# Optimization experiments

Hardware: AMD Instinct MI355X
Metric: run time of the kernel (lower is better)

Reference implementation:

```python
import jax, jax.numpy as jnp
import numpy as np

H2 = 512    # internal hidden = hidden_size*2
E = 128     # embedding_size
V = 50000   # vocabulary_size
L = 512     # max_length (encoder input length)
B = 128     # batch


def setup_inputs() -> dict:
    key = jax.random.key(0)
    ks = jax.random.split(key, 20)
    s = 0.02
    return {
        "input_ids": jax.random.randint(ks[0], (B,), 0, V),
        "hidden": jax.random.normal(ks[1], (1, B, H2), jnp.float32),
        "encoder_outputs": jax.random.normal(ks[2], (L, B, H2), jnp.float32),
        "full_input": jax.random.randint(ks[3], (L, B), 0, V),
        # parameters
        "embedding": jax.random.normal(ks[4], (V, E), jnp.float32) * s,
        "W_ih": jax.random.normal(ks[5], (3 * H2, E), jnp.float32) * s,
        "W_hh": jax.random.normal(ks[6], (3 * H2, H2), jnp.float32) * s,
        "b_ih": jnp.zeros((3 * H2,), jnp.float32),
        "b_hh": jnp.zeros((3 * H2,), jnp.float32),
        "W_ds": jax.random.normal(ks[7], (H2, H2), jnp.float32) * s,
        "b_ds": jnp.zeros((H2,), jnp.float32),
        "w_h": jax.random.normal(ks[8], (H2,), jnp.float32),
        "att_v": jax.random.normal(ks[9], (H2,), jnp.float32),
        "W_oh": jax.random.normal(ks[10], (E, 2 * H2), jnp.float32) * s,
        "b_oh": jnp.zeros((E,), jnp.float32),
        "W_ov": jax.random.normal(ks[11], (V, E), jnp.float32) * s,
        "b_ov": jnp.zeros((V,), jnp.float32),
        "W_ptr": jax.random.normal(ks[12], (1, 2 * H2 + E), jnp.float32) * s,
        "b_ptr": jnp.zeros((1,), jnp.float32),
    }


def reference(input_ids, hidden, encoder_outputs, full_input, embedding,
              W_ih, W_hh, b_ih, b_hh, W_ds, b_ds, w_h, att_v,
              W_oh, b_oh, W_ov, b_ov, W_ptr, b_ptr):
    Bn = input_ids.shape[0]
    Ln = encoder_outputs.shape[0]
    Vn = embedding.shape[0]

    emb = embedding[input_ids]                       # [B, E] (dropout = identity in eval)
    h0 = hidden[0]                                   # [B, 2h]

    # single GRU step (PyTorch gate order r, z, n)
    gx = emb @ W_ih.T + b_ih                         # [B, 3*2h]
    gh = h0 @ W_hh.T + b_hh
    xr, xz, xn = jnp.split(gx, 3, axis=1)
    hr, hz, hn = jnp.split(gh, 3, axis=1)
    r = jax.nn.sigmoid(xr + hr)
    z = jax.nn.sigmoid(xz + hz)
    n = jnp.tanh(xn + r * hn)
    h_new = (1.0 - z) * n + z * h0                   # [B, 2h]

    # Bahdanau-style attention (faithful to source, incl. softmax over dim=1 = batch axis)
    dsl = h_new @ W_ds.T + b_ds                      # [B, 2h]
    att = jnp.tanh(w_h * encoder_outputs + dsl[None])  # [L, B, 2h]
    scores = (att_v * att).sum(-1)                   # [L, B]
    attn = jax.nn.softmax(scores, axis=1)            # torch F.softmax(dim=1)

    context = jnp.einsum('lb,lbh->bh', attn, encoder_outputs)  # [B, 2h]
    combined = jnp.concatenate([h_new, context], axis=1)        # [B, 4h]

    p_vocab = jax.nn.softmax((combined @ W_oh.T + b_oh) @ W_ov.T + b_ov, axis=1)  # [B, V]

    p_gen = jax.nn.sigmoid(jnp.concatenate([combined, emb], axis=1) @ W_ptr.T + b_ptr)  # [B, 1]

    # scatter attention mass onto extended vocab (copy distribution)
    token_input_dist = jnp.zeros((Bn, Vn + Ln), p_vocab.dtype).at[
        jnp.arange(Bn)[:, None], full_input.T
    ].add(attn.T)

    pad = jnp.zeros((Bn, Ln), p_vocab.dtype)
    p_final = jnp.concatenate([p_vocab * p_gen, pad], axis=1) + (1.0 - p_gen) * token_input_dist
    return (p_final, h_new[None], attn)
```

## Files before the change

### kernel.cpp

```cpp
#include <hip/hip_runtime.h>
#include <math.h>

#define B_  128
#define E_  128
#define H2_ 512
#define H3_ 1536
#define L_  512
#define V_  50000
#define VL_ 50512

typedef short bf16x8 __attribute__((ext_vector_type(8)));
typedef float f32x4 __attribute__((ext_vector_type(4)));

__device__ __forceinline__ float fast_tanh(float x) {
    float e = __expf(2.f * x);
    return 1.f - 2.f / (e + 1.f);
}
__device__ __forceinline__ float fast_sigmoid(float x) {
    return 1.f / (1.f + __expf(-x));
}
__device__ __forceinline__ short f2bf(float f) {
    unsigned u = __float_as_uint(f);
    u += 0x7fff + ((u >> 16) & 1);
    return (short)(u >> 16);
}

__global__ void k_init(float* __restrict__ gx, float* __restrict__ gh,
                       float* __restrict__ dsl, float* __restrict__ hid,
                       float* __restrict__ out, float* __restrict__ rsum8,
                       const float* __restrict__ b_ih, const float* __restrict__ b_hh,
                       const float* __restrict__ b_ds, const float* __restrict__ b_oh) {
    int i = blockIdx.x * blockDim.x + threadIdx.x;
    if (i < 196608) { gx[i] = b_ih[i % 1536]; return; }
    i -= 196608;
    if (i < 196608) { gh[i] = b_hh[i % 1536]; return; }
    i -= 196608;
    if (i < 65536)  { dsl[i] = b_ds[i & 511]; return; }
    i -= 65536;
    if (i < 16384)  { hid[i] = b_oh[i & 127]; return; }
    i -= 16384;
    if (i < 65536)  { out[(size_t)(i >> 9) * VL_ + V_ + (i & 511)] = 0.f; return; }
    i -= 65536;
    if (i < 1024)   rsum8[i] = 0.f;
}

__global__ void k_gates(const int* __restrict__ ids, const float* __restrict__ tab,
                        const float* __restrict__ hidden,
                        const float* __restrict__ W_ih, const float* __restrict__ W_hh,
                        float* __restrict__ gx, float* __restrict__ gh) {
    __shared__ float As[32][36];
    __shared__ float Ws[32][36];
    int z = blockIdx.z;
    int which = (z < 2) ? 0 : 1;
    int kbeg  = which ? (z - 2) * 128 : z * 64;
    int kiter = which ? 4 : 2;
    const float* W = which ? W_hh : W_ih;
    int ldw = which ? H2_ : E_;
    float* C = which ? gh : gx;
    int bm = blockIdx.x * 32, bn = blockIdx.y * 32;
    int tid = threadIdx.x;
    int tm0 = (tid / 16) * 2, tn0 = (tid % 16) * 2;
    float acc[2][2] = {};
    for (int it = 0; it < kiter; ++it) {
        int k0 = kbeg + it * 32;
        for (int v = tid; v < 256; v += 256) {
            int m = v >> 3, q = (v & 7) << 2;
            int gm = bm + m;
            const float* arow = which ? (hidden + (size_t)gm * H2_)
                                      : (tab + (size_t)ids[gm] * E_);
            float4 x = *(const float4*)(arow + k0 + q);
            As[q+0][m] = x.x; As[q+1][m] = x.y; As[q+2][m] = x.z; As[q+3][m] = x.w;
        }
        for (int v = tid; v < 256; v += 256) {
            int n = v >> 3, q = (v & 7) << 2;
            float4 x = *(const float4*)(W + (size_t)(bn + n) * ldw + k0 + q);
            Ws[q+0][n] = x.x; Ws[q+1][n] = x.y; Ws[q+2][n] = x.z; Ws[q+3][n] = x.w;
        }
        __syncthreads();
        #pragma unroll
        for (int kk = 0; kk < 32; ++kk) {
            float a0 = As[kk][tm0], a1 = As[kk][tm0+1];
            float w0 = Ws[kk][tn0], w1 = Ws[kk][tn0+1];
            acc[0][0] += a0*w0; acc[0][1] += a0*w1;
            acc[1][0] += a1*w0; acc[1][1] += a1*w1;
        }
        __syncthreads();
    }
    #pragma unroll
    for (int i = 0; i < 2; ++i)
        #pragma unroll
        for (int j = 0; j < 2; ++j)
            atomicAdd(&C[(size_t)(bm+tm0+i) * H3_ + bn+tn0+j], acc[i][j]);
}

template<int BM, int BN, int BK, int TM, int TN, int SPLITK>
__global__ void gemm_t(const float* __restrict__ A, int lda,
                       const float* __restrict__ W, int ldw,
                       float* __restrict__ C, int ldc,
                       int N, int K) {
    __shared__ float As[BK][BM + 4];
    __shared__ float Ws[BK][BN + 4];
    int bm = blockIdx.x * BM, bn = blockIdx.y * BN;
    int tid = threadIdx.x;
    constexpr int NT = BN / TN;
    int tm0 = (tid / NT) * TM;
    int tn0 = (tid % NT) * TN;
    int kchunk = K / SPLITK;
    int kbeg = blockIdx.z * kchunk;
    float acc[TM][TN] = {};
    for (int k0 = kbeg; k0 < kbeg + kchunk; k0 += BK) {
        #pragma unroll
        for (int v = tid; v < BM * BK / 4; v += 256) {
            int m = v / (BK / 4), q = (v % (BK / 4)) * 4;
            float4 x = *(const float4*)(A + (size_t)(bm + m) * lda + k0 + q);
            As[q+0][m] = x.x; As[q+1][m] = x.y; As[q+2][m] = x.z; As[q+3][m] = x.w;
        }
        #pragma unroll
        for (int v = tid; v < BN * BK / 4; v += 256) {
            int n = v / (BK / 4), q = (v % (BK / 4)) * 4;
            float4 x = *(const float4*)(W + (size_t)(bn + n) * ldw + k0 + q);
            Ws[q+0][n] = x.x; Ws[q+1][n] = x.y; Ws[q+2][n] = x.z; Ws[q+3][n] = x.w;
        }
        __syncthreads();
        #pragma unroll
        for (int kk = 0; kk < BK; ++kk) {
            float a[TM], w[TN];
            #pragma unroll
            for (int i = 0; i < TM; ++i) a[i] = As[kk][tm0 + i];
            #pragma unroll
            for (int j = 0; j < TN; ++j) w[j] = Ws[kk][tn0 + j];
            #pragma unroll
            for (int i = 0; i < TM; ++i)
                #pragma unroll
                for (int j = 0; j < TN; ++j) acc[i][j] += a[i] * w[j];
        }
        __syncthreads();
    }
    #pragma unroll
    for (int i = 0; i < TM; ++i)
        #pragma unroll
        for (int j = 0; j < TN; ++j)
            atomicAdd(&C[(size_t)(bm+tm0+i) * ldc + bn+tn0+j], acc[i][j]);
}

__global__ void k_gru(const float* __restrict__ gx, const float* __restrict__ gh,
                      const float* __restrict__ h0,
                      float* __restrict__ comb, float* __restrict__ hout) {
    int idx = blockIdx.x * blockDim.x + threadIdx.x;
    int b = idx >> 9, h = idx & 511;
    const float* gxb = gx + b * H3_;
    const float* ghb = gh + b * H3_;
    float xr = gxb[h], xz = gxb[H2_ + h], xn = gxb[2 * H2_ + h];
    float hr = ghb[h], hz = ghb[H2_ + h], hn = ghb[2 * H2_ + h];
    float r = fast_sigmoid(xr + hr);
    float z = fast_sigmoid(xz + hz);
    float n = fast_tanh(xn + r * hn);
    float hv = (1.f - z) * n + z * h0[idx];
    comb[b * (2 * H2_) + h] = hv;
    comb[b * (2 * H2_) + H2_ + h] = 0.f;
    hout[idx] = hv;
}

__global__ void k_scores(const float* __restrict__ enc, const float* __restrict__ dsl,
                         const float* __restrict__ w_h, const float* __restrict__ att_v,
                         float* __restrict__ scores) {
    int wid = (blockIdx.x << 2) + (threadIdx.x >> 6);
    int lane = threadIdx.x & 63;
    int b = wid & 127, lg = wid >> 7;
    int l0 = lg << 3;
    const float4* d4 = (const float4*)(dsl + b * H2_);
    const float4* w4 = (const float4*)w_h;
    const float4* v4 = (const float4*)att_v;
    float4 d0 = d4[lane], d1 = d4[lane + 64];
    float4 w0 = w4[lane], w1 = w4[lane + 64];
    float4 v0 = v4[lane], v1 = v4[lane + 64];
    float4 e0[8], e1[8];
    #pragma unroll
    for (int q = 0; q < 8; ++q) {
        const float4* e4 = (const float4*)(enc + ((size_t)((l0 + q) * B_ + b)) * H2_);
        e0[q] = e4[lane];
        e1[q] = e4[lane + 64];
    }
    float s[8];
    #pragma unroll
    for (int q = 0; q < 8; ++q) {
        float t;
        t  = v0.x * fast_tanh(w0.x * e0[q].x + d0.x);
        t += v0.y * fast_tanh(w0.y * e0[q].y + d0.y);
        t += v0.z * fast_tanh(w0.z * e0[q].z + d0.z);
        t += v0.w * fast_tanh(w0.w * e0[q].w + d0.w);
        t += v1.x * fast_tanh(w1.x * e1[q].x + d1.x);
        t += v1.y * fast_tanh(w1.y * e1[q].y + d1.y);
        t += v1.z * fast_tanh(w1.z * e1[q].z + d1.z);
        t += v1.w * fast_tanh(w1.w * e1[q].w + d1.w);
        s[q] = t;
    }
    #pragma unroll
    for (int q = 0; q < 8; ++q) {
        float t = s[q];
        #pragma unroll
        for (int o = 32; o; o >>= 1) t += __shfl_xor(t, o);
        if (lane == 0) scores[(l0 + q) * B_ + b] = t;
    }
}

__global__ void k_softmax(const float* __restrict__ scores, float* __restrict__ attn) {
    int l = blockIdx.x, lane = threadIdx.x;
    float s0 = scores[l * B_ + lane], s1 = scores[l * B_ + lane + 64];
    float m = fmaxf(s0, s1);
    #pragma unroll
    for (int o = 32; o; o >>= 1) m = fmaxf(m, __shfl_xor(m, o));
    float e0 = __expf(s0 - m), e1 = __expf(s1 - m);
    float t = e0 + e1;
    #pragma unroll
    for (int o = 32; o; o >>= 1) t += __shfl_xor(t, o);
    float inv = 1.f / t;
    attn[l * B_ + lane] = e0 * inv;
    attn[l * B_ + lane + 64] = e1 * inv;
}

__global__ void k_context(const float* __restrict__ enc, const float* __restrict__ attn,
                          float* __restrict__ comb) {
    int b = blockIdx.x;
    int l0 = blockIdx.y << 6;
    int tid = threadIdx.x;
    __shared__ float a_s[64];
    if (tid < 64) a_s[tid] = attn[(l0 + tid) * B_ + b];
    __syncthreads();
    const float4* e = (const float4*)(enc + ((size_t)l0 * B_ + b) * H2_) + tid;
    float4 c = make_float4(0.f, 0.f, 0.f, 0.f);
    #pragma unroll 8
    for (int i = 0; i < 64; ++i) {
        float4 x = e[(size_t)i * (B_ * H2_ / 4)];
        float a = a_s[i];
        c.x += a * x.x; c.y += a * x.y; c.z += a * x.z; c.w += a * x.w;
    }
    float* dst = comb + b * (2 * H2_) + H2_ + tid * 4;
    atomicAdd(dst + 0, c.x); atomicAdd(dst + 1, c.y);
    atomicAdd(dst + 2, c.z); atomicAdd(dst + 3, c.w);
}

__global__ void k_pgen(const float* __restrict__ comb,
                       const int* __restrict__ ids, const float* __restrict__ tab,
                       const float* __restrict__ W_ptr, const float* __restrict__ b_ptr,
                       float* __restrict__ pgen) {
    int b = blockIdx.x, lane = threadIdx.x;
    float s = 0.f;
    for (int j = lane; j < 2 * H2_; j += 64) s += W_ptr[j] * comb[b * (2 * H2_) + j];
    const float* erow = tab + (size_t)ids[b] * E_;
    for (int j = lane; j < E_; j += 64) s += W_ptr[2 * H2_ + j] * erow[j];
    #pragma unroll
    for (int o = 32; o; o >>= 1) s += __shfl_xor(s, o);
    if (lane == 0) pgen[b] = fast_sigmoid(s + b_ptr[0]);
}

__global__ void k_vocab(const float* __restrict__ hid, const float* __restrict__ Wov,
                        const float* __restrict__ bov, float* __restrict__ out,
                        float* __restrict__ rsum8) {
    __shared__ float sm[4][128];
    int L = threadIdx.x & 63, w = threadIdx.x >> 6;
    int lrow = L & 15, lk = L >> 4;
    int n0 = blockIdx.x * 128 + w * 32;

    bf16x8 bfr[2][4];
    #pragma unroll
    for (int nt = 0; nt < 2; ++nt) {
        int n = n0 + nt * 16 + lrow;
        #pragma unroll
        for (int kk = 0; kk < 4; ++kk) {
            bf16x8 f;
            if (n < V_) {
                const float* p = Wov + (size_t)n * 128 + kk * 32 + lk * 8;
                float4 x = *(const float4*)p, y = *(const float4*)(p + 4);
                f[0]=f2bf(x.x); f[1]=f2bf(x.y); f[2]=f2bf(x.z); f[3]=f2bf(x.w);
                f[4]=f2bf(y.x); f[5]=f2bf(y.y); f[6]=f2bf(y.z); f[7]=f2bf(y.w);
            } else {
                #pragma unroll
                for (int j = 0; j < 8; ++j) f[j] = 0;
            }
            bfr[nt][kk] = f;
        }
    }
    f32x4 acc[8][2] = {};
    #pragma unroll
    for (int mt = 0; mt < 8; ++mt) {
        bf16x8 afr[4];
        #pragma unroll
        for (int kk = 0; kk < 4; ++kk) {
            const float* p = hid + (size_t)(mt * 16 + lrow) * 128 + kk * 32 + lk * 8;
            float4 x = *(const float4*)p, y = *(const float4*)(p + 4);
            bf16x8 f;
            f[0]=f2bf(x.x); f[1]=f2bf(x.y); f[2]=f2bf(x.z); f[3]=f2bf(x.w);
            f[4]=f2bf(y.x); f[5]=f2bf(y.y); f[6]=f2bf(y.z); f[7]=f2bf(y.w);
            afr[kk] = f;
        }
        #pragma unroll
        for (int nt = 0; nt < 2; ++nt)
            #pragma unroll
            for (int kk = 0; kk < 4; ++kk)
                acc[mt][nt] = __builtin_amdgcn_mfma_f32_16x16x32_bf16(
                    afr[kk], bfr[nt][kk], acc[mt][nt], 0, 0, 0);
    }
    float bv[2];
    #pragma unroll
    for (int nt = 0; nt < 2; ++nt) {
        int n = n0 + nt * 16 + lrow;
        bv[nt] = (n < V_) ? bov[n] : 0.f;
    }
    float rs[8][4];
    #pragma unroll
    for (int mt = 0; mt < 8; ++mt) {
        #pragma unroll
        for (int r = 0; r < 4; ++r) rs[mt][r] = 0.f;
        #pragma unroll
        for (int nt = 0; nt < 2; ++nt) {
            int n = n0 + nt * 16 + lrow;
            if (n < V_) {
                #pragma unroll
                for (int r = 0; r < 4; ++r) {
                    int row = mt * 16 + lk * 4 + r;
                    float e = __expf(acc[mt][nt][r] + bv[nt]);
                    out[(size_t)row * VL_ + n] = e;
                    rs[mt][r] += e;
                }
            }
        }
    }
    #pragma unroll
    for (int o = 1; o < 16; o <<= 1)
        #pragma unroll
        for (int mt = 0; mt < 8; ++mt)
            #pragma unroll
            for (int r = 0; r < 4; ++r) rs[mt][r] += __shfl_xor(rs[mt][r], o);
    if (lrow == 0) {
        #pragma unroll
        for (int mt = 0; mt < 8; ++mt)
            #pragma unroll
            for (int r = 0; r < 4; ++r)
                sm[w][mt * 16 + lk * 4 + r] = rs[mt][r];
    }
    __syncthreads();
    if (threadIdx.x < 128) {
        float p = sm[0][threadIdx.x] + sm[1][threadIdx.x]
                + sm[2][threadIdx.x] + sm[3][threadIdx.x];
        atomicAdd(&rsum8[(blockIdx.x & 7) * 128 + threadIdx.x], p);
    }
}

__global__ void k_final(float* __restrict__ out, const float* __restrict__ pgen,
                        const float* __restrict__ rsum8) {
    int b = blockIdx.y, chunk = blockIdx.x, tid = threadIdx.x;
    __shared__ float sc;
    if (tid == 0) {
        float s = 0.f;
        #pragma unroll
        for (int j = 0; j < 8; ++j) s += rsum8[j * 128 + b];
        sc = pgen[b] / s;
    }
    __syncthreads();
    int j = chunk * 256 + tid;
    if (j < V_ / 4) {
        float4* p = (float4*)(out + (size_t)b * VL_) + j;
        float4 x = *p;
        x.x *= sc; x.y *= sc; x.z *= sc; x.w *= sc;
        *p = x;
    }
}

__global__ void k_scatter(float* __restrict__ out, const int* __restrict__ full_input,
                          const float* __restrict__ attn, const float* __restrict__ pgen) {
    int idx = blockIdx.x * blockDim.x + threadIdx.x;
    int b = idx & 127;
    int tok = full_input[idx];
    atomicAdd(&out[(size_t)b * VL_ + tok], (1.f - pgen[b]) * attn[idx]);
}

extern "C" void kernel_launch(void* const* d_in, const int* in_sizes, int n_in,
                              void* d_out, int out_size, void* d_ws, size_t ws_size,
                              hipStream_t stream) {
    const int*   input_ids = (const int*)d_in[0];
    const float* hidden    = (const float*)d_in[1];
    const float* enc       = (const float*)d_in[2];
    const int*   full_in   = (const int*)d_in[3];
    const float* emb_tab   = (const float*)d_in[4];
    const float* W_ih      = (const float*)d_in[5];
    const float* W_hh      = (const float*)d_in[6];
    const float* b_ih      = (const float*)d_in[7];
    const float* b_hh      = (const float*)d_in[8];
    const float* W_ds      = (const float*)d_in[9];
    const float* b_ds      = (const float*)d_in[10];
    const float* w_h       = (const float*)d_in[11];
    const float* att_v     = (const float*)d_in[12];
    const float* W_oh      = (const float*)d_in[13];
    const float* b_oh      = (const float*)d_in[14];
    const float* W_ov      = (const float*)d_in[15];
    const float* b_ov      = (const float*)d_in[16];
    const float* W_ptr     = (const float*)d_in[17];
    const float* b_ptr     = (const float*)d_in[18];

    float* out = (float*)d_out;
    float* p_final = out;
    float* h_out   = out + (size_t)B_ * VL_;
    float* attn    = out + (size_t)B_ * VL_ + B_ * H2_;

    float* ws = (float*)d_ws;
    float* gx     = ws;
    float* gh     = gx + 196608;
    float* comb   = gh + 196608;
    float* dsl    = comb + 131072;
    float* scores = dsl + 65536;
    float* hid    = scores + 65536;
    float* pgen   = hid + 16384;
    float* rsum8  = pgen + 128;

    k_init<<<dim3(2116), dim3(256), 0, stream>>>(gx, gh, dsl, hid, out, rsum8,
                                                 b_ih, b_hh, b_ds, b_oh);
    k_gates<<<dim3(4,48,6), dim3(256), 0, stream>>>(input_ids, emb_tab, hidden,
                                                    W_ih, W_hh, gx, gh);
    k_gru<<<dim3(256), dim3(256), 0, stream>>>(gx, gh, hidden, comb, h_out);
    gemm_t<32,32,32,2,2,4><<<dim3(4,16,4), dim3(256), 0, stream>>>(
        comb, 2*H2_, W_ds, H2_, dsl, H2_, H2_, H2_);
    k_scores<<<dim3(2048), dim3(256), 0, stream>>>(enc, dsl, w_h, att_v, scores);
    k_softmax<<<dim3(L_), dim3(64), 0, stream>>>(scores, attn);
    k_context<<<dim3(B_, 8), dim3(128), 0, stream>>>(enc, attn, comb);
    k_pgen<<<dim3(B_), dim3(64), 0, stream>>>(comb, input_ids, emb_tab, W_ptr, b_ptr, pgen);
    gemm_t<32,32,32,2,2,8><<<dim3(4,4,8), dim3(256), 0, stream>>>(
        comb, 2*H2_, W_oh, 2*H2_, hid, E_, E_, 2*H2_);
    k_vocab<<<dim3(391), dim3(256), 0, stream>>>(hid, W_ov, b_ov, p_final, rsum8);
    k_final<<<dim3(49, 128), dim3(256), 0, stream>>>(p_final, pgen, rsum8);
    k_scatter<<<dim3(L_*B_/256), dim3(256), 0, stream>>>(p_final, full_in, attn, pgen);
}
```

Measured before the change: 146.3 us.

## Replace split-K atomics with partial buffers and recompute vocab logits instead of rescaling

Split-K GEMMs for the gates, the decoder-state projection and the context now write per-split partial buffers with plain stores. Consumers (GRU, scores, a new context+pgen kernel) sum those partials and add the biases, so the init kernel and most atomics go away. The vocab projection is split into two passes: one computes only exp row sums, the other recomputes the logits and writes the normalized, p_gen-scaled output directly. This drops the read-modify-write pass over the 25 MB output in exchange for a second MFMA pass over W_ov, and it enlarges the workspace.

```diff
diff --git a/kernel.cpp b/kernel.cpp
--- a/kernel.cpp
+++ b/kernel.cpp
@@ -25,29 +25,10 @@
     return (short)(u >> 16);
 }
 
-__global__ void k_init(float* __restrict__ gx, float* __restrict__ gh,
-                       float* __restrict__ dsl, float* __restrict__ hid,
-                       float* __restrict__ out, float* __restrict__ rsum8,
-                       const float* __restrict__ b_ih, const float* __restrict__ b_hh,
-                       const float* __restrict__ b_ds, const float* __restrict__ b_oh) {
-    int i = blockIdx.x * blockDim.x + threadIdx.x;
-    if (i < 196608) { gx[i] = b_ih[i % 1536]; return; }
-    i -= 196608;
-    if (i < 196608) { gh[i] = b_hh[i % 1536]; return; }
-    i -= 196608;
-    if (i < 65536)  { dsl[i] = b_ds[i & 511]; return; }
-    i -= 65536;
-    if (i < 16384)  { hid[i] = b_oh[i & 127]; return; }
-    i -= 16384;
-    if (i < 65536)  { out[(size_t)(i >> 9) * VL_ + V_ + (i & 511)] = 0.f; return; }
-    i -= 65536;
-    if (i < 1024)   rsum8[i] = 0.f;
-}
-
 __global__ void k_gates(const int* __restrict__ ids, const float* __restrict__ tab,
                         const float* __restrict__ hidden,
                         const float* __restrict__ W_ih, const float* __restrict__ W_hh,
-                        float* __restrict__ gx, float* __restrict__ gh) {
+                        float* __restrict__ gxp, float* __restrict__ ghp) {
     __shared__ float As[32][36];
     __shared__ float Ws[32][36];
     int z = blockIdx.z;
@@ -56,7 +37,7 @@
     int kiter = which ? 4 : 2;
     const float* W = which ? W_hh : W_ih;
     int ldw = which ? H2_ : E_;
-    float* C = which ? gh : gx;
+    float* C = which ? (ghp + (size_t)(z - 2) * B_ * H3_) : (gxp + (size_t)z * B_ * H3_);
     int bm = blockIdx.x * 32, bn = blockIdx.y * 32;
     int tid = threadIdx.x;
     int tm0 = (tid / 16) * 2, tn0 = (tid % 16) * 2;
@@ -90,14 +71,14 @@
     for (int i = 0; i < 2; ++i)
         #pragma unroll
         for (int j = 0; j < 2; ++j)
-            atomicAdd(&C[(size_t)(bm+tm0+i) * H3_ + bn+tn0+j], acc[i][j]);
-}
-
-template<int BM, int BN, int BK, int TM, int TN, int SPLITK>
+            C[(size_t)(bm+tm0+i) * H3_ + bn+tn0+j] = acc[i][j];
+}
+
+template<int BM, int BN, int BK, int TM, int TN, int SPLITK, bool ATOMIC>
 __global__ void gemm_t(const float* __restrict__ A, int lda,
                        const float* __restrict__ W, int ldw,
                        float* __restrict__ C, int ldc,
-                       int N, int K) {
+                       int N, int K, int partElems) {
     __shared__ float As[BK][BM + 4];
     __shared__ float Ws[BK][BN + 4];
     int bm = blockIdx.x * BM, bn = blockIdx.y * BN;
@@ -136,42 +117,63 @@
         }
         __syncthreads();
     }
+    float* Cz = ATOMIC ? C : (C + (size_t)blockIdx.z * partElems);
     #pragma unroll
     for (int i = 0; i < TM; ++i)
         #pragma unroll
-        for (int j = 0; j < TN; ++j)
-            atomicAdd(&C[(size_t)(bm+tm0+i) * ldc + bn+tn0+j], acc[i][j]);
-}
-
-__global__ void k_gru(const float* __restrict__ gx, const float* __restrict__ gh,
-                      const float* __restrict__ h0,
-                      float* __restrict__ comb, float* __restrict__ hout) {
+        for (int j = 0; j < TN; ++j) {
+            if (ATOMIC) atomicAdd(&Cz[(size_t)(bm+tm0+i) * ldc + bn+tn0+j], acc[i][j]);
+            else        Cz[(size_t)(bm+tm0+i) * ldc + bn+tn0+j] = acc[i][j];
+        }
+}
+
+__global__ void k_gru(const float* __restrict__ gxp, const float* __restrict__ ghp,
+                      const float* __restrict__ b_ih, const float* __restrict__ b_hh,
+                      const float* __restrict__ h0, const float* __restrict__ b_oh,
+                      float* __restrict__ comb, float* __restrict__ hout,
+                      float* __restrict__ hid, float* __restrict__ rsum8) {
     int idx = blockIdx.x * blockDim.x + threadIdx.x;
     int b = idx >> 9, h = idx & 511;
-    const float* gxb = gx + b * H3_;
-    const float* ghb = gh + b * H3_;
-    float xr = gxb[h], xz = gxb[H2_ + h], xn = gxb[2 * H2_ + h];
-    float hr = ghb[h], hz = ghb[H2_ + h], hn = ghb[2 * H2_ + h];
+    const float* gx0 = gxp + (size_t)b * H3_;
+    const float* gx1 = gx0 + (size_t)B_ * H3_;
+    float xr = gx0[h]         + gx1[h]         + b_ih[h];
+    float xz = gx0[H2_+h]     + gx1[H2_+h]     + b_ih[H2_+h];
+    float xn = gx0[2*H2_+h]   + gx1[2*H2_+h]   + b_ih[2*H2_+h];
+    float hr = b_hh[h], hz = b_hh[H2_+h], hn = b_hh[2*H2_+h];
+    #pragma unroll
+    for (int z = 0; z < 4; ++z) {
+        const float* g = ghp + ((size_t)z * B_ + b) * H3_;
+        hr += g[h]; hz += g[H2_+h]; hn += g[2*H2_+h];
+    }
     float r = fast_sigmoid(xr + hr);
-    float z = fast_sigmoid(xz + hz);
+    float zz = fast_sigmoid(xz + hz);
     float n = fast_tanh(xn + r * hn);
-    float hv = (1.f - z) * n + z * h0[idx];
+    float hv = (1.f - zz) * n + zz * h0[idx];
     comb[b * (2 * H2_) + h] = hv;
-    comb[b * (2 * H2_) + H2_ + h] = 0.f;
     hout[idx] = hv;
-}
-
-__global__ void k_scores(const float* __restrict__ enc, const float* __restrict__ dsl,
+    if (idx < B_ * E_) hid[idx] = b_oh[idx & 127];
+    if (idx < 1024)    rsum8[idx] = 0.f;
+}
+
+__global__ void k_scores(const float* __restrict__ enc, const float* __restrict__ dslp,
+                         const float* __restrict__ b_ds,
                          const float* __restrict__ w_h, const float* __restrict__ att_v,
                          float* __restrict__ scores) {
     int wid = (blockIdx.x << 2) + (threadIdx.x >> 6);
     int lane = threadIdx.x & 63;
     int b = wid & 127, lg = wid >> 7;
     int l0 = lg << 3;
-    const float4* d4 = (const float4*)(dsl + b * H2_);
     const float4* w4 = (const float4*)w_h;
     const float4* v4 = (const float4*)att_v;
-    float4 d0 = d4[lane], d1 = d4[lane + 64];
+    const float4* bd4 = (const float4*)b_ds;
+    float4 d0 = bd4[lane], d1 = bd4[lane + 64];
+    #pragma unroll
+    for (int z = 0; z < 4; ++z) {
+        const float4* dp = (const float4*)(dslp + (size_t)z * B_ * H2_ + b * H2_);
+        float4 p0 = dp[lane], p1 = dp[lane + 64];
+        d0.x += p0.x; d0.y += p0.y; d0.z += p0.z; d0.w += p0.w;
+        d1.x += p1.x; d1.y += p1.y; d1.z += p1.z; d1.w += p1.w;
+    }
     float4 w0 = w4[lane], w1 = w4[lane + 64];
     float4 v0 = v4[lane], v1 = v4[lane + 64];
     float4 e0[8], e1[8];
@@ -220,7 +222,7 @@
 }
 
 __global__ void k_context(const float* __restrict__ enc, const float* __restrict__ attn,
-                          float* __restrict__ comb) {
+                          float* __restrict__ ctxp) {
     int b = blockIdx.x;
     int l0 = blockIdx.y << 6;
     int tid = threadIdx.x;
@@ -235,28 +237,45 @@
         float a = a_s[i];
         c.x += a * x.x; c.y += a * x.y; c.z += a * x.z; c.w += a * x.w;
     }
-    float* dst = comb + b * (2 * H2_) + H2_ + tid * 4;
-    atomicAdd(dst + 0, c.x); atomicAdd(dst + 1, c.y);
-    atomicAdd(dst + 2, c.z); atomicAdd(dst + 3, c.w);
-}
-
-__global__ void k_pgen(const float* __restrict__ comb,
-                       const int* __restrict__ ids, const float* __restrict__ tab,
-                       const float* __restrict__ W_ptr, const float* __restrict__ b_ptr,
-                       float* __restrict__ pgen) {
-    int b = blockIdx.x, lane = threadIdx.x;
-    float s = 0.f;
-    for (int j = lane; j < 2 * H2_; j += 64) s += W_ptr[j] * comb[b * (2 * H2_) + j];
-    const float* erow = tab + (size_t)ids[b] * E_;
-    for (int j = lane; j < E_; j += 64) s += W_ptr[2 * H2_ + j] * erow[j];
-    #pragma unroll
-    for (int o = 32; o; o >>= 1) s += __shfl_xor(s, o);
-    if (lane == 0) pgen[b] = fast_sigmoid(s + b_ptr[0]);
-}
-
-__global__ void k_vocab(const float* __restrict__ hid, const float* __restrict__ Wov,
-                        const float* __restrict__ bov, float* __restrict__ out,
-                        float* __restrict__ rsum8) {
+    ((float4*)(ctxp + ((size_t)blockIdx.y * B_ + b) * H2_))[tid] = c;
+}
+
+__global__ void k_ctxpgen(const float* __restrict__ ctxp, const int* __restrict__ ids,
+                          const float* __restrict__ tab, const float* __restrict__ W_ptr,
+                          const float* __restrict__ b_ptr,
+                          float* __restrict__ comb, float* __restrict__ pgen) {
+    __shared__ float red[128];
+    int b = blockIdx.x, tid = threadIdx.x;
+    float4 c = make_float4(0.f, 0.f, 0.f, 0.f);
+    #pragma unroll
+    for (int z = 0; z < 8; ++z) {
+        float4 x = ((const float4*)(ctxp + ((size_t)z * B_ + b) * H2_))[tid];
+        c.x += x.x; c.y += x.y; c.z += x.z; c.w += x.w;
+    }
+    ((float4*)(comb + b * (2 * H2_) + H2_))[tid] = c;
+    const float4* wp = (const float4*)W_ptr;
+    float4 wc = wp[128 + tid];
+    float s = c.x * wc.x + c.y * wc.y + c.z * wc.z + c.w * wc.w;
+    float4 hv = ((const float4*)(comb + b * (2 * H2_)))[tid];
+    float4 wh = wp[tid];
+    s += hv.x * wh.x + hv.y * wh.y + hv.z * wh.z + hv.w * wh.w;
+    if (tid < 32) {
+        float4 ev = ((const float4*)(tab + (size_t)ids[b] * E_))[tid];
+        float4 we = wp[256 + tid];
+        s += ev.x * we.x + ev.y * we.y + ev.z * we.z + ev.w * we.w;
+    }
+    red[tid] = s;
+    __syncthreads();
+    if (tid < 64) {
+        float t = red[tid] + red[tid + 64];
+        #pragma unroll
+        for (int o = 32; o; o >>= 1) t += __shfl_xor(t, o);
+        if (tid == 0) pgen[b] = fast_sigmoid(t + b_ptr[0]);
+    }
+}
+
+__global__ void k_vsum(const float* __restrict__ hid, const float* __restrict__ Wov,
+                       const float* __restrict__ bov, float* __restrict__ rsum8) {
     __shared__ float sm[4][128];
     int L = threadIdx.x & 63, w = threadIdx.x >> 6;
     int lrow = L & 15, lk = L >> 4;
@@ -317,12 +336,8 @@
             int n = n0 + nt * 16 + lrow;
             if (n < V_) {
                 #pragma unroll
-                for (int r = 0; r < 4; ++r) {
-                    int row = mt * 16 + lk * 4 + r;
-                    float e = __expf(acc[mt][nt][r] + bv[nt]);
-                    out[(size_t)row * VL_ + n] = e;
-                    rs[mt][r] += e;
-                }
+                for (int r = 0; r < 4; ++r)
+                    rs[mt][r] += __expf(acc[mt][nt][r] + bv[nt]);
             }
         }
     }
@@ -347,23 +362,87 @@
     }
 }
 
-__global__ void k_final(float* __restrict__ out, const float* __restrict__ pgen,
-                        const float* __restrict__ rsum8) {
-    int b = blockIdx.y, chunk = blockIdx.x, tid = threadIdx.x;
-    __shared__ float sc;
-    if (tid == 0) {
+__global__ void k_vwrite(const float* __restrict__ hid, const float* __restrict__ Wov,
+                         const float* __restrict__ bov, const float* __restrict__ pgen,
+                         const float* __restrict__ rsum8, float* __restrict__ out) {
+    __shared__ float scs[128];
+    if (blockIdx.x == 391) {
+        for (int i = threadIdx.x; i < B_ * (L_ / 4); i += 256) {
+            int b = i >> 7, k = i & 127;
+            ((float4*)(out + (size_t)b * VL_ + V_))[k] = make_float4(0.f,0.f,0.f,0.f);
+        }
+        return;
+    }
+    if (threadIdx.x < 128) {
         float s = 0.f;
         #pragma unroll
-        for (int j = 0; j < 8; ++j) s += rsum8[j * 128 + b];
-        sc = pgen[b] / s;
+        for (int j = 0; j < 8; ++j) s += rsum8[j * 128 + threadIdx.x];
+        scs[threadIdx.x] = pgen[threadIdx.x] / s;
     }
     __syncthreads();
-    int j = chunk * 256 + tid;
-    if (j < V_ / 4) {
-        float4* p = (float4*)(out + (size_t)b * VL_) + j;
-        float4 x = *p;
-        x.x *= sc; x.y *= sc; x.z *= sc; x.w *= sc;
-        *p = x;
+    int L = threadIdx.x & 63, w = threadIdx.x >> 6;
+    int lrow = L & 15, lk = L >> 4;
+    int n0 = blockIdx.x * 128 + w * 32;
+
+    bf16x8 bfr[2][4];
+    #pragma unroll
+    for (int nt = 0; nt < 2; ++nt) {
+        int n = n0 + nt * 16 + lrow;
+        #pragma unroll
+        for (int kk = 0; kk < 4; ++kk) {
+            bf16x8 f;
+            if (n < V_) {
+                const float* p = Wov + (size_t)n * 128 + kk * 32 + lk * 8;
+                float4 x = *(const float4*)p, y = *(const float4*)(p + 4);
+                f[0]=f2bf(x.x); f[1]=f2bf(x.y); f[2]=f2bf(x.z); f[3]=f2bf(x.w);
+                f[4]=f2bf(y.x); f[5]=f2bf(y.y); f[6]=f2bf(y.z); f[7]=f2bf(y.w);
+            } else {
+                #pragma unroll
+                for (int j = 0; j < 8; ++j) f[j] = 0;
+            }
+            bfr[nt][kk] = f;
+        }
+    }
+    f32x4 acc[8][2] = {};
+    #pragma unroll
+    for (int mt = 0; mt < 8; ++mt) {
+        bf16x8 afr[4];
+        #pragma unroll
+        for (int kk = 0; kk < 4; ++kk) {
+            const float* p = hid + (size_t)(mt * 16 + lrow) * 128 + kk * 32 + lk * 8;
+            float4 x = *(const float4*)p, y = *(const float4*)(p + 4);
+            bf16x8 f;
+            f[0]=f2bf(x.x); f[1]=f2bf(x.y); f[2]=f2bf(x.z); f[3]=f2bf(x.w);
+            f[4]=f2bf(y.x); f[5]=f2bf(y.y); f[6]=f2bf(y.z); f[7]=f2bf(y.w);
+            afr[kk] = f;
+        }
+        #pragma unroll
+        for (int nt = 0; nt < 2; ++nt)
+            #pragma unroll
+            for (int kk = 0; kk < 4; ++kk)
+                acc[mt][nt] = __builtin_amdgcn_mfma_f32_16x16x32_bf16(
+                    afr[kk], bfr[nt][kk], acc[mt][nt], 0, 0, 0);
+    }
+    float bv[2];
+    #pragma unroll
+    for (int nt = 0; nt < 2; ++nt) {
+        int n = n0 + nt * 16 + lrow;
+        bv[nt] = (n < V_) ? bov[n] : 0.f;
+    }
+    #pragma unroll
+    for (int mt = 0; mt < 8; ++mt) {
+        #pragma unroll
+        for (int nt = 0; nt < 2; ++nt) {
+            int n = n0 + nt * 16 + lrow;
+            if (n < V_) {
+                #pragma unroll
+                for (int r = 0; r < 4; ++r) {
+                    int row = mt * 16 + lk * 4 + r;
+                    out[(size_t)row * VL_ + n] =
+                        __expf(acc[mt][nt][r] + bv[nt]) * scs[row];
+                }
+            }
+        }
     }
 }
 
@@ -404,29 +483,30 @@
     float* attn    = out + (size_t)B_ * VL_ + B_ * H2_;
 
     float* ws = (float*)d_ws;
-    float* gx     = ws;
-    float* gh     = gx + 196608;
-    float* comb   = gh + 196608;
-    float* dsl    = comb + 131072;
-    float* scores = dsl + 65536;
-    float* hid    = scores + 65536;
+    float* gxp    = ws;
+    float* ghp    = gxp + 393216;
+    float* comb   = ghp + 786432;
+    float* dslp   = comb + 131072;
+    float* scores = dslp + 262144;
+    float* ctxp   = scores + 65536;
+    float* hid    = ctxp + 524288;
     float* pgen   = hid + 16384;
     float* rsum8  = pgen + 128;
 
-    k_init<<<dim3(2116), dim3(256), 0, stream>>>(gx, gh, dsl, hid, out, rsum8,
-                                                 b_ih, b_hh, b_ds, b_oh);
     k_gates<<<dim3(4,48,6), dim3(256), 0, stream>>>(input_ids, emb_tab, hidden,
-                                                    W_ih, W_hh, gx, gh);
-    k_gru<<<dim3(256), dim3(256), 0, stream>>>(gx, gh, hidden, comb, h_out);
-    gemm_t<32,32,32,2,2,4><<<dim3(4,16,4), dim3(256), 0, stream>>>(
-        comb, 2*H2_, W_ds, H2_, dsl, H2_, H2_, H2_);
-    k_scores<<<dim3(2048), dim3(256), 0, stream>>>(enc, dsl, w_h, att_v, scores);
+                                                    W_ih, W_hh, gxp, ghp);
+    k_gru<<<dim3(256), dim3(256), 0, stream>>>(gxp, ghp, b_ih, b_hh, hidden, b_oh,
+                                               comb, h_out, hid, rsum8);
+    gemm_t<32,32,32,2,2,4,false><<<dim3(4,16,4), dim3(256), 0, stream>>>(
+        comb, 2*H2_, W_ds, H2_, dslp, H2_, H2_, H2_, B_*H2_);
+    k_scores<<<dim3(2048), dim3(256), 0, stream>>>(enc, dslp, b_ds, w_h, att_v, scores);
     k_softmax<<<dim3(L_), dim3(64), 0, stream>>>(scores, attn);
-    k_context<<<dim3(B_, 8), dim3(128), 0, stream>>>(enc, attn, comb);
-    k_pgen<<<dim3(B_), dim3(64), 0, stream>>>(comb, input_ids, emb_tab, W_ptr, b_ptr, pgen);
-    gemm_t<32,32,32,2,2,8><<<dim3(4,4,8), dim3(256), 0, stream>>>(
-        comb, 2*H2_, W_oh, 2*H2_, hid, E_, E_, 2*H2_);
-    k_vocab<<<dim3(391), dim3(256), 0, stream>>>(hid, W_ov, b_ov, p_final, rsum8);
-    k_final<<<dim3(49, 128), dim3(256), 0, stream>>>(p_final, pgen, rsum8);
+    k_context<<<dim3(B_, 8), dim3(128), 0, stream>>>(enc, attn, ctxp);
+    k_ctxpgen<<<dim3(B_), dim3(128), 0, stream>>>(ctxp, input_ids, emb_tab,
+                                                  W_ptr, b_ptr, comb, pgen);
+    gemm_t<32,32,32,2,2,8,true><<<dim3(4,4,8), dim3(256), 0, stream>>>(
+        comb, 2*H2_, W_oh, 2*H2_, hid, E_, E_, 2*H2_, 0);
+    k_vsum<<<dim3(391), dim3(256), 0, stream>>>(hid, W_ov, b_ov, rsum8);
+    k_vwrite<<<dim3(392), dim3(256), 0, stream>>>(hid, W_ov, b_ov, pgen, rsum8, p_final);
     k_scatter<<<dim3(L_*B_/256), dim3(256), 0, stream>>>(p_final, full_in, attn, pgen);
 }
```

Measured after the change: 140.6 us, median of 2. 1.04x faster.
